# Kernel tuning notes

Measured on AMD Instinct MI355X. Metric: run time of the kernel, lower is better.

## Reference

```python
import jax, jax.numpy as jnp
import numpy as np

B, S, D = 4, 2048, 768
LN_EPS = 1e-12


def setup_inputs() -> dict:
    key = jax.random.key(0)
    k0, k1, k2, k3 = jax.random.split(key, 4)
    scale = 1.0 / np.sqrt(D).astype(np.float32)
    return {
        "hidden_states": jax.random.normal(k0, (B, S, D), jnp.float32),
        "attention_mask": jnp.ones((B, 1, S, S), jnp.int32),
        "prior_n_attn": jax.random.uniform(k1, (B, S, S), jnp.float32),
        "ln_w": jnp.ones((D,), jnp.float32),
        "ln_b": jnp.zeros((D,), jnp.float32),
        "wq": jax.random.normal(k2, (D, D), jnp.float32) * scale,
        "bq": jnp.zeros((D,), jnp.float32),
        "wk": jax.random.normal(k3, (D, D), jnp.float32) * scale,
        "bk": jnp.zeros((D,), jnp.float32),
    }


def reference(hidden_states, attention_mask, prior_n_attn, ln_w, ln_b, wq, bq, wk, bk):
    _, S_, D_ = hidden_states.shape
    # LayerNorm (biased variance, as torch.nn.LayerNorm)
    mu = hidden_states.mean(-1, keepdims=True)
    var = ((hidden_states - mu) ** 2).mean(-1, keepdims=True)
    h = (hidden_states - mu) / jnp.sqrt(var + LN_EPS) * ln_w + ln_b

    a = jnp.eye(S_, k=1, dtype=jnp.int32)      # superdiagonal
    bI = jnp.eye(S_, dtype=jnp.int32)          # diagonal
    c = jnp.eye(S_, k=-1, dtype=jnp.int32)     # subdiagonal
    tri = jnp.triu(jnp.ones((S_, S_), jnp.float32))

    # mask & (a + c): band of width 1 off the diagonal; then squeeze dim 1
    mask = (attention_mask.astype(jnp.int32) & (a + c))[:, 0]  # [B,S,S]

    q = h @ wq + bq
    k = h @ wk + bk
    scores = jnp.einsum("bsd,btd->bst", q, k) / D_
    scores = jnp.where(mask == 0, -jnp.inf, scores)
    n = jnp.nan_to_num(jax.nn.softmax(scores, axis=-1))
    n = jnp.sqrt(n * jnp.swapaxes(n, -2, -1) + 1e-9)
    n = prior_n_attn + (1.0 - prior_n_attn) * n

    # keep only the superdiagonal of log(n + 1e-9); zero elsewhere
    logm = jnp.log(n + 1e-9) * a.astype(n.dtype)
    # prefix-sum via triangular matmuls (same math as torch source)
    t = logm @ tri                                   # [B,S,S]
    g = jnp.exp(jnp.einsum("ij,bjk->bik", tri, t))   # [B,S,S]
    su = tri - bI.astype(tri.dtype)                  # strictly-upper indicator
    g = g * su                                       # masked_fill((tri-b)==0, 0)
    diag_part = jnp.where(bI == 0, 1e-9, n)          # n.masked_fill(b==0, 1e-9)
    g = g + jnp.swapaxes(g, -2, -1) + diag_part
    return (g, n)
```

## Files before the change

### kernel.cpp

```cpp
#include <hip/hip_runtime.h>
#include <hip/hip_bf16.h>
#include <math.h>
#include <stdint.h>

#define BB 4
#define SS 2048
#define DD 768
#define MM (BB*SS)

typedef __attribute__((ext_vector_type(4))) float  f32x4;
typedef __attribute__((ext_vector_type(8))) __bf16 bf16x8;
typedef __attribute__((ext_vector_type(4))) __bf16 bf16x4;

#define AS1 __attribute__((address_space(1)))
#define AS3 __attribute__((address_space(3)))

__global__ __launch_bounds__(256) void combined_kernel(
        const float* __restrict__ x, const float* __restrict__ lw,
        const float* __restrict__ lb, const float* __restrict__ wq,
        const float* __restrict__ wk, const float* __restrict__ bq,
        const float* __restrict__ bk, __bf16* __restrict__ G,
        float* __restrict__ u, float* __restrict__ v, float* __restrict__ cb,
        __bf16* __restrict__ h) {
    __shared__ __attribute__((aligned(16))) __bf16 As[64][32];
    __shared__ __attribute__((aligned(16))) __bf16 Bs[64][32];
    const int bid = blockIdx.x;
    if (bid >= 529) {
        const int row = (bid - 529) * 4 + (threadIdx.x >> 6);
        const int lane = threadIdx.x & 63;
        const float* xr = x + (size_t)row * DD + lane * 12;
        f32x4 a0 = *(const f32x4*)(xr), a1 = *(const f32x4*)(xr + 4), a2 = *(const f32x4*)(xr + 8);
        float xs[12];
#pragma unroll
        for (int c = 0; c < 4; c++) { xs[c] = a0[c]; xs[4 + c] = a1[c]; xs[8 + c] = a2[c]; }
        float s = 0.f, ss = 0.f;
#pragma unroll
        for (int c = 0; c < 12; c++) { s += xs[c]; ss += xs[c] * xs[c]; }
#pragma unroll
        for (int o = 1; o < 64; o <<= 1) { s += __shfl_xor(s, o); ss += __shfl_xor(ss, o); }
        const float mu = s * (1.0f / DD);
        const float var = ss * (1.0f / DD) - mu * mu;
        const float rstd = 1.0f / sqrtf(var + 1e-12f);
        const float* wp = lw + lane * 12; const float* bp = lb + lane * 12;
        f32x4 w0 = *(const f32x4*)(wp), w1 = *(const f32x4*)(wp + 4), w2 = *(const f32x4*)(wp + 8);
        f32x4 b0 = *(const f32x4*)(bp), b1 = *(const f32x4*)(bp + 4), b2 = *(const f32x4*)(bp + 8);
        bf16x4 o0, o1, o2;
#pragma unroll
        for (int c = 0; c < 4; c++) {
            o0[c] = (__bf16)((xs[c]     - mu) * rstd * w0[c] + b0[c]);
            o1[c] = (__bf16)((xs[4 + c] - mu) * rstd * w1[c] + b1[c]);
            o2[c] = (__bf16)((xs[8 + c] - mu) * rstd * w2[c] + b2[c]);
        }
        __bf16* hr = h + (size_t)row * DD + lane * 12;
        *(bf16x4*)(hr) = o0; *(bf16x4*)(hr + 4) = o1; *(bf16x4*)(hr + 8) = o2;
        return;
    }
    if (bid >= 144) {
        const int id = bid - 144;
        const int lane = threadIdx.x & 63, wv_ = threadIdx.x >> 6;
        if (id == 384) {
            if (wv_ != 0) return;
            float s = 0.f;
#pragma unroll
            for (int m = 0; m < 12; m++) s += bq[lane + 64 * m] * bk[lane + 64 * m];
#pragma unroll
            for (int o = 1; o < 64; o <<= 1) s += __shfl_xor(s, o);
            if (lane == 0) cb[0] = s;
            return;
        }
        const bool isU = id < 192;
        const int row = (isU ? id : id - 192) * 4 + wv_;
        const float* W = isU ? wq : wk;
        const float* bvec = isU ? bk : bq;
        const float* wr_ = W + (size_t)row * DD;
        float s = 0.f;
#pragma unroll
        for (int m = 0; m < 12; m++) s += wr_[lane + 64 * m] * bvec[lane + 64 * m];
#pragma unroll
        for (int o = 1; o < 64; o <<= 1) s += __shfl_xor(s, o);
        if (lane == 0) (isU ? u : v)[row] = s;
        return;
    }
    const int m0 = (bid % 12) * 64;
    const int n0 = (bid / 12) * 64;
    const int t = threadIdx.x;
    const int wave = t >> 6, lane = t & 63;
    const int wr = wave >> 1, wc = wave & 1;
    const int srow = t >> 2, scol = (t & 3) * 8;
    f32x4 acc[2][2] = {};

    for (int k0 = 0; k0 < DD; k0 += 32) {
        const float* ga = wq + (size_t)(m0 + srow) * DD + k0 + scol;
        const float* gb = wk + (size_t)(n0 + srow) * DD + k0 + scol;
        f32x4 a0 = *(const f32x4*)(ga), a1 = *(const f32x4*)(ga + 4);
        f32x4 b0 = *(const f32x4*)(gb), b1 = *(const f32x4*)(gb + 4);
        bf16x8 av, bv;
#pragma unroll
        for (int c = 0; c < 4; c++) {
            av[c] = (__bf16)a0[c]; av[4 + c] = (__bf16)a1[c];
            bv[c] = (__bf16)b0[c]; bv[4 + c] = (__bf16)b1[c];
        }
        __syncthreads();
        *(bf16x8*)&As[srow][scol] = av;
        *(bf16x8*)&Bs[srow][scol] = bv;
        __syncthreads();
        const int r = lane & 15, ko = (lane >> 4) << 3;
        bf16x8 af[2], bvf[2];
#pragma unroll
        for (int i = 0; i < 2; i++) af[i]  = *(const bf16x8*)&As[wr * 32 + i * 16 + r][ko];
#pragma unroll
        for (int j = 0; j < 2; j++) bvf[j] = *(const bf16x8*)&Bs[wc * 32 + j * 16 + r][ko];
#pragma unroll
        for (int i = 0; i < 2; i++)
#pragma unroll
            for (int j = 0; j < 2; j++)
                acc[i][j] = __builtin_amdgcn_mfma_f32_16x16x32_bf16(af[i], bvf[j], acc[i][j], 0, 0, 0);
    }
#pragma unroll
    for (int i = 0; i < 2; i++) {
        const int mm = m0 + wr * 32 + i * 16 + (lane >> 4) * 4;
#pragma unroll
        for (int j = 0; j < 2; j++) {
            const int nn = n0 + wc * 32 + j * 16 + (lane & 15);
#pragma unroll
            for (int rr = 0; rr < 4; rr++)
                G[(size_t)(mm + rr) * DD + nn] = (__bf16)acc[i][j][rr];
        }
    }
}

__global__ __launch_bounds__(256) void rgemm_kernel(const __bf16* __restrict__ A,
        const __bf16* __restrict__ Bt, const float* __restrict__ u,
        __bf16* __restrict__ C) {
    __shared__ __attribute__((aligned(16))) __bf16 As[128][32];
    __shared__ __attribute__((aligned(16))) __bf16 Bs[128][32];
    const int m0 = blockIdx.y * 128;
    const int n0 = blockIdx.x * 128;
    const int t = threadIdx.x;
    const int wave = t >> 6, lane = t & 63;
    const int wr = wave >> 1, wc = wave & 1;
    f32x4 acc[4][4] = {};

    char* asb = (char*)&As[0][0];
    char* bsb = (char*)&Bs[0][0];
    const int c0  = wave * 64 + lane;
    const int rA0 = c0 >> 2;
    const int cA0 = (c0 & 3) << 3;

    for (int k0 = 0; k0 < DD; k0 += 32) {
        const __bf16* ga0 = A  + (size_t)(m0 + rA0) * DD + k0 + cA0;
        const __bf16* ga1 = ga0 + (size_t)64 * DD;
        const __bf16* gb0 = Bt + (size_t)(n0 + rA0) * DD + k0 + cA0;
        const __bf16* gb1 = gb0 + (size_t)64 * DD;
        __builtin_amdgcn_global_load_lds((const AS1 void*)(ga0), (AS3 void*)(asb + wave * 1024),        16, 0, 0);
        __builtin_amdgcn_global_load_lds((const AS1 void*)(ga1), (AS3 void*)(asb + 4096 + wave * 1024), 16, 0, 0);
        __builtin_amdgcn_global_load_lds((const AS1 void*)(gb0), (AS3 void*)(bsb + wave * 1024),        16, 0, 0);
        __builtin_amdgcn_global_load_lds((const AS1 void*)(gb1), (AS3 void*)(bsb + 4096 + wave * 1024), 16, 0, 0);
        __syncthreads();
        const int r = lane & 15, ko = (lane >> 4) << 3;
        bf16x8 af[4], bvf[4];
#pragma unroll
        for (int i = 0; i < 4; i++) af[i]  = *(const bf16x8*)&As[wr * 64 + i * 16 + r][ko];
#pragma unroll
        for (int j = 0; j < 4; j++) bvf[j] = *(const bf16x8*)&Bs[wc * 64 + j * 16 + r][ko];
#pragma unroll
        for (int i = 0; i < 4; i++)
#pragma unroll
            for (int j = 0; j < 4; j++)
                acc[i][j] = __builtin_amdgcn_mfma_f32_16x16x32_bf16(af[i], bvf[j], acc[i][j], 0, 0, 0);
        __syncthreads();
    }
#pragma unroll
    for (int i = 0; i < 4; i++) {
        const int mm = m0 + wr * 64 + i * 16 + (lane >> 4) * 4;
#pragma unroll
        for (int j = 0; j < 4; j++) {
            const int nn = n0 + wc * 64 + j * 16 + (lane & 15);
            const float bias = u[nn];
#pragma unroll
            for (int rr = 0; rr < 4; rr++)
                C[(size_t)(mm + rr) * DD + nn] = (__bf16)(acc[i][j][rr] + bias);
        }
    }
}

__global__ __launch_bounds__(256) void band_kernel(const __bf16* __restrict__ h,
        const __bf16* __restrict__ R, const int* __restrict__ att,
        const float* __restrict__ v, const float* __restrict__ cbp,
        const float* __restrict__ prior,
        float* __restrict__ du_o, float* __restrict__ dn_o, float* __restrict__ w_o,
        int* __restrict__ fl_o, float* __restrict__ prsup) {
    const int idx  = blockIdx.x * 4 + (threadIdx.x >> 6);
    const int lane = threadIdx.x & 63;
    const int b = idx >> 11;
    const int s = idx & 2047;
    if (lane == 1 && s < SS - 1)
        prsup[idx] = prior[((size_t)b * SS + s) * SS + s + 1];
    const __bf16* hp = h + (size_t)idx * DD + lane * 12;
    bf16x4 h0 = *(const bf16x4*)(hp), h1 = *(const bf16x4*)(hp + 4), h2 = *(const bf16x4*)(hp + 8);
    float hv[12];
#pragma unroll
    for (int c = 0; c < 4; c++) { hv[c] = (float)h0[c]; hv[4 + c] = (float)h1[c]; hv[8 + c] = (float)h2[c]; }
    const float* vp = v + lane * 12;
    f32x4 v0 = *(const f32x4*)(vp), v1 = *(const f32x4*)(vp + 4), v2 = *(const f32x4*)(vp + 8);
    float du = 0.f, dn = 0.f, w = 0.f;
#pragma unroll
    for (int c = 0; c < 4; c++) {
        w += hv[c] * v0[c] + hv[4 + c] * v1[c] + hv[8 + c] * v2[c];
    }
    if (s < SS - 1) {
        const __bf16* rp = R + (size_t)(idx + 1) * DD + lane * 12;
        bf16x4 r0 = *(const bf16x4*)(rp), r1 = *(const bf16x4*)(rp + 4), r2 = *(const bf16x4*)(rp + 8);
#pragma unroll
        for (int c = 0; c < 4; c++)
            du += hv[c] * (float)r0[c] + hv[4 + c] * (float)r1[c] + hv[8 + c] * (float)r2[c];
    }
    if (s > 0) {
        const __bf16* rp = R + (size_t)(idx - 1) * DD + lane * 12;
        bf16x4 r0 = *(const bf16x4*)(rp), r1 = *(const bf16x4*)(rp + 4), r2 = *(const bf16x4*)(rp + 8);
#pragma unroll
        for (int c = 0; c < 4; c++)
            dn += hv[c] * (float)r0[c] + hv[4 + c] * (float)r1[c] + hv[8 + c] * (float)r2[c];
    }
#pragma unroll
    for (int o = 1; o < 64; o <<= 1) {
        du += __shfl_xor(du, o); dn += __shfl_xor(dn, o); w += __shfl_xor(w, o);
    }
    if (lane == 0) {
        const bool au = (s < SS - 1) && ((att[((size_t)b * SS + s) * SS + (s + 1)] & 1) != 0);
        const bool ad = (s > 0)      && ((att[((size_t)b * SS + s) * SS + (s - 1)] & 1) != 0);
        du_o[idx] = du;
        dn_o[idx] = dn;
        w_o[idx]  = w + cbp[0];
        fl_o[idx] = (au ? 1 : 0) | (ad ? 2 : 0);
    }
}

__global__ __launch_bounds__(256) void scan_kernel(const float* __restrict__ du_i,
        const float* __restrict__ dn_i, const float* __restrict__ w_i,
        const int* __restrict__ fl_i, const float* __restrict__ prsup,
        float* __restrict__ nb, double* __restrict__ P2) {
    const int b = blockIdx.x;
    const int t = threadIdx.x;
    __shared__ float sh_pd[SS];
    __shared__ double warr[256];
    float pu_r[8];
#pragma unroll
    for (int e = 0; e < 8; e++) {
        const int s = t * 8 + e;
        const int idx = b * SS + s;
        const int fl = fl_i[idx];
        const bool au = fl & 1, ad = fl & 2;
        float puv = 0.f, pdv = 0.f;
        if (au || ad) {
            const float eu = au ? (du_i[idx] + w_i[idx + 1]) * (1.0f / DD) : 0.f;
            const float ed = ad ? (dn_i[idx] + w_i[idx - 1]) * (1.0f / DD) : 0.f;
            float mx = au ? eu : ed;
            if (au && ad) mx = fmaxf(eu, ed);
            const float zu = au ? expf(eu - mx) : 0.f;
            const float zd = ad ? expf(ed - mx) : 0.f;
            const float iz = 1.f / (zu + zd);
            puv = zu * iz; pdv = zd * iz;
        }
        pu_r[e] = puv;
        sh_pd[s] = pdv;
    }
    __syncthreads();
    double L[8];
    double mysum = 0.0;
#pragma unroll
    for (int e = 0; e < 8; e++) {
        const int s = t * 8 + e;
        double Lv = 0.0;
        float nbv = 0.f;
        if (s < SS - 1) {
            nbv = sqrtf(pu_r[e] * sh_pd[s + 1] + 1e-9f);
            const float pr = prsup[b * SS + s];
            const float nsup = pr + (1.f - pr) * nbv;
            Lv = (double)log2f(nsup + 1e-9f);
        }
        nb[b * SS + s] = nbv;
        L[e] = Lv; mysum += Lv;
    }
    warr[t] = mysum;
    __syncthreads();
    for (int o = 1; o < 256; o <<= 1) {
        double vv = 0.0;
        if (t >= o) vv = warr[t - o];
        __syncthreads();
        if (t >= o) warr[t] += vv;
        __syncthreads();
    }
    double run = warr[t] - mysum;
#pragma unroll
    for (int e = 0; e < 8; e++) {
        P2[(size_t)b * SS + t * 8 + e] = run;
        run += L[e];
    }
}

__global__ __launch_bounds__(256) void out_kernel(const float* __restrict__ prior,
        const float* __restrict__ nb, const double* __restrict__ P2,
        float* __restrict__ gout, float* __restrict__ nout) {
    const size_t t8 = (size_t)blockIdx.x * 256 + threadIdx.x;
    const int b = (int)(t8 >> 19);
    const size_t off = t8 << 3;
    const size_t r = off & ((1u << 22) - 1);
    const int i  = (int)(r >> 11);
    const int k0 = (int)(r & 2047);
    const f32x4 p0 = *(const f32x4*)(prior + off);
    const f32x4 p1 = *(const f32x4*)(prior + off + 4);
    const double* Pb = P2 + ((size_t)b << 11);
    const double Pi = Pb[i];
    const float* nbb = nb + ((size_t)b << 11);
    f32x4 g0, g1, n0, n1;
#pragma unroll
    for (int c = 0; c < 8; c++) {
        const int k = k0 + c;
        const float pr = (c < 4) ? p0[c] : p1[c - 4];
        float vv = 3.16227766016838e-5f;
        if (k == i + 1)      vv = nbb[i];
        else if (k == i - 1) vv = nbb[k];
        const float nval = pr + (1.f - pr) * vv;
        float g;
        if (k == i) {
            g = nval;
        } else {
            const double Pk = Pb[k];
            const double dd = (k > i) ? (Pk - Pi) : (Pi - Pk);
            g = exp2f((float)dd) + 1e-9f;
        }
        if (c < 4) { g0[c] = g; n0[c] = nval; }
        else       { g1[c - 4] = g; n1[c - 4] = nval; }
    }
    *(f32x4*)(gout + off)     = g0;
    *(f32x4*)(gout + off + 4) = g1;
    *(f32x4*)(nout + off)     = n0;
    *(f32x4*)(nout + off + 4) = n1;
}

extern "C" void kernel_launch(void* const* d_in, const int* in_sizes, int n_in,
                              void* d_out, int out_size, void* d_ws, size_t ws_size,
                              hipStream_t stream) {
    const float* hs    = (const float*)d_in[0];
    const int*   att   = (const int*)d_in[1];
    const float* prior = (const float*)d_in[2];
    const float* ln_w  = (const float*)d_in[3];
    const float* ln_b  = (const float*)d_in[4];
    const float* wq    = (const float*)d_in[5];
    const float* bq    = (const float*)d_in[6];
    const float* wk    = (const float*)d_in[7];
    const float* bk    = (const float*)d_in[8];

    float* gout = (float*)d_out;
    float* nout = gout + (size_t)BB * SS * SS;

    char* ws = (char*)d_ws;
    __bf16* h     = (__bf16*)(ws);
    __bf16* G     = (__bf16*)(ws + 12582912);
    __bf16* R     = (__bf16*)(ws + 13762560);
    float*  u     = (float*) (ws + 26345472);
    float*  v     = (float*) (ws + 26348544);
    float*  cbp   = (float*) (ws + 26351616);
    float*  du    = (float*) (ws + 26351872);
    float*  dn    = (float*) (ws + 26384640);
    float*  wv    = (float*) (ws + 26417408);
    int*    fl    = (int*)   (ws + 26450176);
    float*  prsup = (float*) (ws + 26482944);
    float*  nbuf  = (float*) (ws + 26515712);
    double* P2    = (double*)(ws + 26548480);

    combined_kernel<<<dim3(2577), dim3(256), 0, stream>>>(hs, ln_w, ln_b, wq, wk, bq, bk, G, u, v, cbp, h);
    rgemm_kernel<<<dim3(6, MM / 128), dim3(256), 0, stream>>>(h, G, u, R);
    band_kernel<<<dim3(MM / 4), dim3(256), 0, stream>>>(h, R, att, v, cbp, prior, du, dn, wv, fl, prsup);
    scan_kernel<<<dim3(BB), dim3(256), 0, stream>>>(du, dn, wv, fl, prsup, nbuf, P2);
    out_kernel<<<dim3((BB * SS * SS / 8) / 256), dim3(256), 0, stream>>>(prior, nbuf, P2, gout, nout);
}
```

Before: 106.5 us.

## Fuse band dot-products into rgemm epilogue and drop intermediate R buffer

The rgemm kernel no longer writes the bf16 product matrix R. Its epilogue now directly forms each row's dot products with the neighbouring h rows and with v, and writes per-column-slot partial sums that the scan kernel reduces. This removes the band kernel launch and the full write and re-read of R. The attention-flag and prior-superdiagonal gathers move into extra blocks of the combined kernel. In exchange the rgemm tile shrinks to 64x128, the epilogue does scattered scalar bf16 loads of h, and the four-block scan kernel takes on a 12-way partial-sum reduction.

```diff
diff --git a/kernel.cpp b/kernel.cpp
--- a/kernel.cpp
+++ b/kernel.cpp
@@ -19,12 +19,23 @@
         const float* __restrict__ x, const float* __restrict__ lw,
         const float* __restrict__ lb, const float* __restrict__ wq,
         const float* __restrict__ wk, const float* __restrict__ bq,
-        const float* __restrict__ bk, __bf16* __restrict__ G,
+        const float* __restrict__ bk, const int* __restrict__ att,
+        const float* __restrict__ prior, __bf16* __restrict__ G,
         float* __restrict__ u, float* __restrict__ v, float* __restrict__ cb,
-        __bf16* __restrict__ h) {
+        __bf16* __restrict__ h, int* __restrict__ fl, float* __restrict__ prsup) {
     __shared__ __attribute__((aligned(16))) __bf16 As[64][32];
     __shared__ __attribute__((aligned(16))) __bf16 Bs[64][32];
     const int bid = blockIdx.x;
+    if (bid >= 2577) {
+        const int idx = (bid - 2577) * 256 + threadIdx.x;
+        const int b = idx >> 11, s = idx & 2047;
+        const bool au = (s < SS - 1) && ((att[((size_t)b * SS + s) * SS + (s + 1)] & 1) != 0);
+        const bool ad = (s > 0)      && ((att[((size_t)b * SS + s) * SS + (s - 1)] & 1) != 0);
+        fl[idx] = (au ? 1 : 0) | (ad ? 2 : 0);
+        if (s < SS - 1)
+            prsup[idx] = prior[((size_t)b * SS + s) * SS + s + 1];
+        return;
+    }
     if (bid >= 529) {
         const int row = (bid - 529) * 4 + (threadIdx.x >> 6);
         const int lane = threadIdx.x & 63;
@@ -131,130 +142,117 @@
 
 __global__ __launch_bounds__(256) void rgemm_kernel(const __bf16* __restrict__ A,
         const __bf16* __restrict__ Bt, const float* __restrict__ u,
-        __bf16* __restrict__ C) {
-    __shared__ __attribute__((aligned(16))) __bf16 As[128][32];
+        const float* __restrict__ v, float* __restrict__ du_part,
+        float* __restrict__ dn_part, float* __restrict__ w_part) {
+    __shared__ __attribute__((aligned(16))) __bf16 As[64][32];
     __shared__ __attribute__((aligned(16))) __bf16 Bs[128][32];
-    const int m0 = blockIdx.y * 128;
-    const int n0 = blockIdx.x * 128;
+    const int bid = blockIdx.x;
+    const int mt = bid & 127, nt = bid >> 7;
+    const int m0 = mt * 64, n0 = nt * 128;
     const int t = threadIdx.x;
     const int wave = t >> 6, lane = t & 63;
     const int wr = wave >> 1, wc = wave & 1;
-    f32x4 acc[4][4] = {};
+    f32x4 acc[2][4] = {};
 
     char* asb = (char*)&As[0][0];
     char* bsb = (char*)&Bs[0][0];
-    const int c0  = wave * 64 + lane;
-    const int rA0 = c0 >> 2;
-    const int cA0 = (c0 & 3) << 3;
+    const int rA = (wave << 4) + (lane >> 2);
+    const int cA = (lane & 3) << 3;
 
     for (int k0 = 0; k0 < DD; k0 += 32) {
-        const __bf16* ga0 = A  + (size_t)(m0 + rA0) * DD + k0 + cA0;
-        const __bf16* ga1 = ga0 + (size_t)64 * DD;
-        const __bf16* gb0 = Bt + (size_t)(n0 + rA0) * DD + k0 + cA0;
+        const __bf16* ga  = A  + (size_t)(m0 + rA) * DD + k0 + cA;
+        const __bf16* gb0 = Bt + (size_t)(n0 + rA) * DD + k0 + cA;
         const __bf16* gb1 = gb0 + (size_t)64 * DD;
-        __builtin_amdgcn_global_load_lds((const AS1 void*)(ga0), (AS3 void*)(asb + wave * 1024),        16, 0, 0);
-        __builtin_amdgcn_global_load_lds((const AS1 void*)(ga1), (AS3 void*)(asb + 4096 + wave * 1024), 16, 0, 0);
+        __builtin_amdgcn_global_load_lds((const AS1 void*)(ga),  (AS3 void*)(asb + wave * 1024),        16, 0, 0);
         __builtin_amdgcn_global_load_lds((const AS1 void*)(gb0), (AS3 void*)(bsb + wave * 1024),        16, 0, 0);
         __builtin_amdgcn_global_load_lds((const AS1 void*)(gb1), (AS3 void*)(bsb + 4096 + wave * 1024), 16, 0, 0);
         __syncthreads();
         const int r = lane & 15, ko = (lane >> 4) << 3;
-        bf16x8 af[4], bvf[4];
-#pragma unroll
-        for (int i = 0; i < 4; i++) af[i]  = *(const bf16x8*)&As[wr * 64 + i * 16 + r][ko];
+        bf16x8 af[2], bvf[4];
+#pragma unroll
+        for (int i = 0; i < 2; i++) af[i]  = *(const bf16x8*)&As[wr * 32 + i * 16 + r][ko];
 #pragma unroll
         for (int j = 0; j < 4; j++) bvf[j] = *(const bf16x8*)&Bs[wc * 64 + j * 16 + r][ko];
 #pragma unroll
-        for (int i = 0; i < 4; i++)
+        for (int i = 0; i < 2; i++)
 #pragma unroll
             for (int j = 0; j < 4; j++)
                 acc[i][j] = __builtin_amdgcn_mfma_f32_16x16x32_bf16(af[i], bvf[j], acc[i][j], 0, 0, 0);
         __syncthreads();
     }
-#pragma unroll
-    for (int i = 0; i < 4; i++) {
-        const int mm = m0 + wr * 64 + i * 16 + (lane >> 4) * 4;
-#pragma unroll
-        for (int j = 0; j < 4; j++) {
-            const int nn = n0 + wc * 64 + j * 16 + (lane & 15);
-            const float bias = u[nn];
-#pragma unroll
-            for (int rr = 0; rr < 4; rr++)
-                C[(size_t)(mm + rr) * DD + nn] = (__bf16)(acc[i][j][rr] + bias);
-        }
-    }
-}
-
-__global__ __launch_bounds__(256) void band_kernel(const __bf16* __restrict__ h,
-        const __bf16* __restrict__ R, const int* __restrict__ att,
-        const float* __restrict__ v, const float* __restrict__ cbp,
-        const float* __restrict__ prior,
-        float* __restrict__ du_o, float* __restrict__ dn_o, float* __restrict__ w_o,
-        int* __restrict__ fl_o, float* __restrict__ prsup) {
-    const int idx  = blockIdx.x * 4 + (threadIdx.x >> 6);
-    const int lane = threadIdx.x & 63;
-    const int b = idx >> 11;
-    const int s = idx & 2047;
-    if (lane == 1 && s < SS - 1)
-        prsup[idx] = prior[((size_t)b * SS + s) * SS + s + 1];
-    const __bf16* hp = h + (size_t)idx * DD + lane * 12;
-    bf16x4 h0 = *(const bf16x4*)(hp), h1 = *(const bf16x4*)(hp + 4), h2 = *(const bf16x4*)(hp + 8);
-    float hv[12];
-#pragma unroll
-    for (int c = 0; c < 4; c++) { hv[c] = (float)h0[c]; hv[4 + c] = (float)h1[c]; hv[8 + c] = (float)h2[c]; }
-    const float* vp = v + lane * 12;
-    f32x4 v0 = *(const f32x4*)(vp), v1 = *(const f32x4*)(vp + 4), v2 = *(const f32x4*)(vp + 8);
-    float du = 0.f, dn = 0.f, w = 0.f;
-#pragma unroll
-    for (int c = 0; c < 4; c++) {
-        w += hv[c] * v0[c] + hv[4 + c] * v1[c] + hv[8 + c] * v2[c];
-    }
-    if (s < SS - 1) {
-        const __bf16* rp = R + (size_t)(idx + 1) * DD + lane * 12;
-        bf16x4 r0 = *(const bf16x4*)(rp), r1 = *(const bf16x4*)(rp + 4), r2 = *(const bf16x4*)(rp + 8);
-#pragma unroll
-        for (int c = 0; c < 4; c++)
-            du += hv[c] * (float)r0[c] + hv[4 + c] * (float)r1[c] + hv[8 + c] * (float)r2[c];
-    }
-    if (s > 0) {
-        const __bf16* rp = R + (size_t)(idx - 1) * DD + lane * 12;
-        bf16x4 r0 = *(const bf16x4*)(rp), r1 = *(const bf16x4*)(rp + 4), r2 = *(const bf16x4*)(rp + 8);
-#pragma unroll
-        for (int c = 0; c < 4; c++)
-            dn += hv[c] * (float)r0[c] + hv[4 + c] * (float)r1[c] + hv[8 + c] * (float)r2[c];
-    }
-#pragma unroll
-    for (int o = 1; o < 64; o <<= 1) {
-        du += __shfl_xor(du, o); dn += __shfl_xor(dn, o); w += __shfl_xor(w, o);
-    }
-    if (lane == 0) {
-        const bool au = (s < SS - 1) && ((att[((size_t)b * SS + s) * SS + (s + 1)] & 1) != 0);
-        const bool ad = (s > 0)      && ((att[((size_t)b * SS + s) * SS + (s - 1)] & 1) != 0);
-        du_o[idx] = du;
-        dn_o[idx] = dn;
-        w_o[idx]  = w + cbp[0];
-        fl_o[idx] = (au ? 1 : 0) | (ad ? 2 : 0);
-    }
-}
-
-__global__ __launch_bounds__(256) void scan_kernel(const float* __restrict__ du_i,
-        const float* __restrict__ dn_i, const float* __restrict__ w_i,
-        const int* __restrict__ fl_i, const float* __restrict__ prsup,
+    int colg[4]; float ub[4], vb[4];
+#pragma unroll
+    for (int j = 0; j < 4; j++) {
+        colg[j] = n0 + wc * 64 + j * 16 + (lane & 15);
+        ub[j] = u[colg[j]];
+        vb[j] = v[colg[j]];
+    }
+    const int slot = nt * 2 + wc;
+#pragma unroll
+    for (int i = 0; i < 2; i++) {
+#pragma unroll
+        for (int rr = 0; rr < 4; rr++) {
+            const int row = m0 + wr * 32 + i * 16 + (lane >> 4) * 4 + rr;
+            const int rm = (row == 0) ? 0 : row - 1;
+            const int rp = (row == MM - 1) ? MM - 1 : row + 1;
+            const __bf16* hm = A + (size_t)rm * DD;
+            const __bf16* hz = A + (size_t)row * DD;
+            const __bf16* hp = A + (size_t)rp * DD;
+            float dua = 0.f, dna = 0.f, wa = 0.f;
+#pragma unroll
+            for (int j = 0; j < 4; j++) {
+                const float Rv = acc[i][j][rr] + ub[j];
+                dua += Rv * (float)hm[colg[j]];
+                dna += Rv * (float)hp[colg[j]];
+                wa  += vb[j] * (float)hz[colg[j]];
+            }
+#pragma unroll
+            for (int o = 1; o < 16; o <<= 1) {
+                dua += __shfl_xor(dua, o);
+                dna += __shfl_xor(dna, o);
+                wa  += __shfl_xor(wa, o);
+            }
+            if ((lane & 15) == 0) {
+                du_part[slot * MM + row] = dua;
+                dn_part[slot * MM + row] = dna;
+                w_part [slot * MM + row] = wa;
+            }
+        }
+    }
+}
+
+__global__ __launch_bounds__(256) void scan_kernel(const float* __restrict__ du_part,
+        const float* __restrict__ dn_part, const float* __restrict__ w_part,
+        const float* __restrict__ cbp, const int* __restrict__ fl_i,
+        const float* __restrict__ prsup,
         float* __restrict__ nb, double* __restrict__ P2) {
     const int b = blockIdx.x;
     const int t = threadIdx.x;
-    __shared__ float sh_pd[SS];
+    __shared__ float du_s[SS], dn_s[SS], w_s[SS], sh_pd[SS];
     __shared__ double warr[256];
+    for (int x = t; x < SS; x += 256) {
+        const int idx = b * SS + x;
+        float d1 = 0.f, d2 = 0.f, d3 = 0.f;
+#pragma unroll
+        for (int p = 0; p < 12; p++) {
+            d1 += du_part[p * MM + idx];
+            d2 += dn_part[p * MM + idx];
+            d3 += w_part [p * MM + idx];
+        }
+        du_s[x] = d1; dn_s[x] = d2; w_s[x] = d3;
+    }
+    __syncthreads();
+    const float cb = cbp[0];
     float pu_r[8];
 #pragma unroll
     for (int e = 0; e < 8; e++) {
         const int s = t * 8 + e;
-        const int idx = b * SS + s;
-        const int fl = fl_i[idx];
+        const int fl = fl_i[b * SS + s];
         const bool au = fl & 1, ad = fl & 2;
         float puv = 0.f, pdv = 0.f;
         if (au || ad) {
-            const float eu = au ? (du_i[idx] + w_i[idx + 1]) * (1.0f / DD) : 0.f;
-            const float ed = ad ? (dn_i[idx] + w_i[idx - 1]) * (1.0f / DD) : 0.f;
+            const float eu = au ? (du_s[s + 1] + w_s[s + 1] + cb) * (1.0f / DD) : 0.f;
+            const float ed = ad ? (dn_s[s - 1] + w_s[s - 1] + cb) * (1.0f / DD) : 0.f;
             float mx = au ? eu : ed;
             if (au && ad) mx = fmaxf(eu, ed);
             const float zu = au ? expf(eu - mx) : 0.f;
@@ -356,23 +354,22 @@
     float* nout = gout + (size_t)BB * SS * SS;
 
     char* ws = (char*)d_ws;
-    __bf16* h     = (__bf16*)(ws);
-    __bf16* G     = (__bf16*)(ws + 12582912);
-    __bf16* R     = (__bf16*)(ws + 13762560);
-    float*  u     = (float*) (ws + 26345472);
-    float*  v     = (float*) (ws + 26348544);
-    float*  cbp   = (float*) (ws + 26351616);
-    float*  du    = (float*) (ws + 26351872);
-    float*  dn    = (float*) (ws + 26384640);
-    float*  wv    = (float*) (ws + 26417408);
-    int*    fl    = (int*)   (ws + 26450176);
-    float*  prsup = (float*) (ws + 26482944);
-    float*  nbuf  = (float*) (ws + 26515712);
-    double* P2    = (double*)(ws + 26548480);
-
-    combined_kernel<<<dim3(2577), dim3(256), 0, stream>>>(hs, ln_w, ln_b, wq, wk, bq, bk, G, u, v, cbp, h);
-    rgemm_kernel<<<dim3(6, MM / 128), dim3(256), 0, stream>>>(h, G, u, R);
-    band_kernel<<<dim3(MM / 4), dim3(256), 0, stream>>>(h, R, att, v, cbp, prior, du, dn, wv, fl, prsup);
-    scan_kernel<<<dim3(BB), dim3(256), 0, stream>>>(du, dn, wv, fl, prsup, nbuf, P2);
+    __bf16* h       = (__bf16*)(ws);
+    __bf16* G       = (__bf16*)(ws + 12582912);
+    float*  u       = (float*) (ws + 13762560);
+    float*  v       = (float*) (ws + 13765632);
+    float*  cbp     = (float*) (ws + 13768704);
+    int*    fl      = (int*)   (ws + 13768960);
+    float*  prsup   = (float*) (ws + 13801728);
+    float*  du_part = (float*) (ws + 13834496);
+    float*  dn_part = (float*) (ws + 14227712);
+    float*  w_part  = (float*) (ws + 14620928);
+    float*  nbuf    = (float*) (ws + 15014144);
+    double* P2      = (double*)(ws + 15046912);
+
+    combined_kernel<<<dim3(2609), dim3(256), 0, stream>>>(hs, ln_w, ln_b, wq, wk, bq, bk,
+                                                          att, prior, G, u, v, cbp, h, fl, prsup);
+    rgemm_kernel<<<dim3(768), dim3(256), 0, stream>>>(h, G, u, v, du_part, dn_part, w_part);
+    scan_kernel<<<dim3(BB), dim3(256), 0, stream>>>(du_part, dn_part, w_part, cbp, fl, prsup, nbuf, P2);
     out_kernel<<<dim3((BB * SS * SS / 8) / 256), dim3(256), 0, stream>>>(prior, nbuf, P2, gout, nout);
 }
```

After: 100.4 us. 1.06x faster.
